# Kernel tuning notes

Hardware: AMD Instinct MI355X
Metric: run time of the kernel (lower is better)

The kernel has to match this reference:

```python
import jax, jax.numpy as jnp
import numpy as np

N = 50000      # ncount
IN_CH = 256    # in_channels
OUT_CH = 128   # out_channels
NNZ = 800000   # nnz per sparse matrix (avg degree 16)


def _spmm(rows, cols, vals, dense, n_rows):
    # sparse(COO) @ dense : gather rows of dense by col index, scale, scatter-add by row
    contrib = vals[:, None] * dense[cols]              # [nnz, F]
    return jax.ops.segment_sum(contrib, rows, num_segments=n_rows)


def setup_inputs() -> dict:
    key = jax.random.key(0)
    ks = jax.random.split(key, 12)
    phi_indices = jnp.stack([
        jax.random.randint(ks[0], (NNZ,), 0, N),
        jax.random.randint(ks[1], (NNZ,), 0, N)])
    phi_values = jax.random.normal(ks[2], (NNZ,), dtype=jnp.float32)
    phi_inverse_indices = jnp.stack([
        jax.random.randint(ks[3], (NNZ,), 0, N),
        jax.random.randint(ks[4], (NNZ,), 0, N)])
    phi_inverse_values = jax.random.normal(ks[5], (NNZ,), dtype=jnp.float32)
    feature_indices = jnp.stack([
        jax.random.randint(ks[6], (NNZ,), 0, N),       # node index
        jax.random.randint(ks[7], (NNZ,), 0, IN_CH)])  # feature column
    feature_values = jax.random.normal(ks[8], (NNZ,), dtype=jnp.float32)
    # xavier_uniform for weight_matrix
    limit = float(np.sqrt(6.0 / (IN_CH + OUT_CH)))
    weight_matrix = jax.random.uniform(ks[9], (IN_CH, OUT_CH), jnp.float32, -limit, limit)
    # diagonal filter Theta init uniform(0.9, 1.1)
    diagonal_weight_filter = jax.random.uniform(ks[10], (N,), jnp.float32, 0.9, 1.1)
    return {
        "phi_indices": phi_indices,
        "phi_values": phi_values,
        "phi_inverse_indices": phi_inverse_indices,
        "phi_inverse_values": phi_inverse_values,
        "feature_indices": feature_indices,
        "feature_values": feature_values,
        "weight_matrix": weight_matrix,
        "diagonal_weight_filter": diagonal_weight_filter,
        "dropout": 0,
    }


def reference(phi_indices, phi_values, phi_inverse_indices, phi_inverse_values,
              feature_indices, feature_values, weight_matrix,
              diagonal_weight_filter, dropout):
    # rescaled_phi = phi @ diag(theta): scales column j of phi by theta[j]
    scaled_phi_vals = phi_values * diagonal_weight_filter[phi_indices[1]]
    # filtered = features(sparse N x IN) @ W  -> [N, OUT]
    filtered = _spmm(feature_indices[0], feature_indices[1], feature_values,
                     weight_matrix, N)
    # (phi * D * phi_inv) @ filtered computed associatively without dense N x N:
    tmp = _spmm(phi_inverse_indices[0], phi_inverse_indices[1],
                phi_inverse_values, filtered, N)              # phi_inv @ filtered
    localized = _spmm(phi_indices[0], phi_indices[1],
                      scaled_phi_vals, tmp, N)                # (phi D) @ tmp
    # dropout in eval mode (training=False) is identity
    return jax.nn.relu(localized)
```

## Files before the change

### kernel.cpp

```cpp
#include <hip/hip_runtime.h>
#include <hip/hip_fp16.h>


#define OUT_CH 128
#define HALF_CH 64
#define RPB 256
#define RPB_SHIFT 8
#define MAX_NB 256
#define EPB 4096
#define MAX_CHUNK 16


__global__ __launch_bounds__(256) void bucket_hist_kernel(
    const int* __restrict__ rows0, int n0,
    const int* __restrict__ rows1, int n1,
    const int* __restrict__ rows2, int n2,
    int* __restrict__ hist_part,
    int NB, int NBLK)
{
    int m = blockIdx.y;
    const int* rows = (m == 0) ? rows0 : (m == 1) ? rows1 : rows2;
    int nnz         = (m == 0) ? n0    : (m == 1) ? n1    : n2;
    __shared__ int bins[MAX_NB];
    if (threadIdx.x < NB) bins[threadIdx.x] = 0;
    __syncthreads();
    int base = blockIdx.x * EPB;
    #pragma unroll 4
    for (int k = 0; k < EPB / 256; ++k) {
        int i = base + k * 256 + threadIdx.x;
        if (i < nnz) atomicAdd(&bins[rows[i] >> RPB_SHIFT], 1);
    }
    __syncthreads();
    int* out = hist_part + ((size_t)(m * NBLK + blockIdx.x)) * NB;
    if (threadIdx.x < NB) out[threadIdx.x] = bins[threadIdx.x];
}


__global__ __launch_bounds__(256) void scan_blocks_wave_kernel(
    int* __restrict__ hist_part, int* __restrict__ totals, int NB, int NBLK)
{
    int w = blockIdx.x * 4 + (threadIdx.x >> 6);
    if (w >= 3 * NB) return;
    int lane = threadIdx.x & 63;
    int m = w / NB, b = w - m * NB;
    const int chunk = (NBLK + 63) >> 6;
    int base_blk = lane * chunk;

    int v[MAX_CHUNK];
    int sum = 0;
    for (int k = 0; k < chunk; ++k) {
        int blk = base_blk + k;
        int x = (blk < NBLK) ? hist_part[((size_t)(m * NBLK + blk)) * NB + b] : 0;
        v[k] = x; sum += x;
    }
    int incl = sum;
    #pragma unroll
    for (int s = 1; s < 64; s <<= 1) {
        int y = __shfl_up(incl, s);
        if (lane >= s) incl += y;
    }
    int run = incl - sum;
    for (int k = 0; k < chunk; ++k) {
        int blk = base_blk + k;
        if (blk < NBLK) {
            hist_part[((size_t)(m * NBLK + blk)) * NB + b] = run;
            run += v[k];
        }
    }
    if (lane == 63) totals[w] = incl;
}


__global__ __launch_bounds__(1024) void scan_buckets_kernel(
    const int* __restrict__ totals, int* __restrict__ bases, int NB)
{
    int m = blockIdx.x;
    int t = threadIdx.x;
    int x = (t < NB) ? totals[m * NB + t] : 0;
    int lane = t & 63, wid = t >> 6;
    int incl = x;
    #pragma unroll
    for (int s = 1; s < 64; s <<= 1) {
        int y = __shfl_up(incl, s);
        if (lane >= s) incl += y;
    }
    __shared__ int wtot[16];
    __shared__ int wbase[16];
    if (lane == 63) wtot[wid] = incl;
    __syncthreads();
    if (t == 0) {
        int run = 0;
        #pragma unroll
        for (int w = 0; w < 16; ++w) { int v = wtot[w]; wbase[w] = run; run += v; }
    }
    __syncthreads();
    if (t < NB) bases[m * NB + t] = wbase[wid] + incl - x;
}


__global__ __launch_bounds__(256) void bucket_scatter_kernel(
    const int* __restrict__ rows0, const int* __restrict__ cols0, const float* __restrict__ vals0, int n0,
    const int* __restrict__ rows1, const int* __restrict__ cols1, const float* __restrict__ vals1, int n1,
    const int* __restrict__ rows2, const int* __restrict__ cols2, const float* __restrict__ vals2, int n2,
    const float* __restrict__ theta,
    const int* __restrict__ hist_part, const int* __restrict__ bases,
    int2* __restrict__ eb0, int2* __restrict__ eb1, int2* __restrict__ eb2,
    int NB, int NBLK)
{
    int m = blockIdx.y;
    const int* rows; const int* cols; const float* vals; int nnz; int2* eb;
    if (m == 0)      { rows = rows0; cols = cols0; vals = vals0; nnz = n0; eb = eb0; }
    else if (m == 1) { rows = rows1; cols = cols1; vals = vals1; nnz = n1; eb = eb1; }
    else             { rows = rows2; cols = cols2; vals = vals2; nnz = n2; eb = eb2; }

    __shared__ int cur[MAX_NB];
    const int* hp = hist_part + ((size_t)(m * NBLK + blockIdx.x)) * NB;
    const int* bs = bases + m * NB;
    if (threadIdx.x < NB) cur[threadIdx.x] = bs[threadIdx.x] + hp[threadIdx.x];
    __syncthreads();

    int base = blockIdx.x * EPB;
    bool fold = (m == 2);
    #pragma unroll 4
    for (int k = 0; k < EPB / 256; ++k) {
        int i = base + k * 256 + threadIdx.x;
        if (i < nnz) {
            int r = rows[i], c = cols[i];
            float v = vals[i];
            if (fold) v *= theta[c];
            int pos = atomicAdd(&cur[r >> RPB_SHIFT], 1);
            eb[pos] = make_int2(c | ((r & (RPB - 1)) << 16), __float_as_int(v));
        }
    }
}


__global__ __launch_bounds__(256) void bucket_to_csr_kernel(
    const int2* __restrict__ eb0, const int2* __restrict__ eb1, const int2* __restrict__ eb2,
    int2* __restrict__ ec0, int2* __restrict__ ec1, int2* __restrict__ ec2,
    const int* __restrict__ bases,
    int* __restrict__ off,
    int n0, int n1, int n2, int NB, int n)
{
    int m = blockIdx.y;
    int b = blockIdx.x;
    const int2* eb; int2* ec; int nnz;
    if (m == 0)      { eb = eb0; ec = ec0; nnz = n0; }
    else if (m == 1) { eb = eb1; ec = ec1; nnz = n1; }
    else             { eb = eb2; ec = ec2; nnz = n2; }
    int base = bases[m * NB + b];
    int end  = (b + 1 < NB) ? bases[m * NB + b + 1] : nnz;

    __shared__ int hist[RPB];
    __shared__ int cur[RPB];
    __shared__ int loc[RPB + 1];
    __shared__ int wtot[4];
    __shared__ int wbase[4];
    int t = threadIdx.x;
    hist[t] = 0; cur[t] = 0;
    __syncthreads();
    for (int i = base + t; i < end; i += 256)
        atomicAdd(&hist[(eb[i].x >> 16) & (RPB - 1)], 1);
    __syncthreads();
    {
        int x = hist[t];
        int lane = t & 63, wid = t >> 6;
        int incl = x;
        #pragma unroll
        for (int s = 1; s < 64; s <<= 1) {
            int y = __shfl_up(incl, s);
            if (lane >= s) incl += y;
        }
        if (lane == 63) wtot[wid] = incl;
        __syncthreads();
        if (t == 0) {
            int run = 0;
            #pragma unroll
            for (int w = 0; w < 4; ++w) { int v = wtot[w]; wbase[w] = run; run += v; }
        }
        __syncthreads();
        loc[t] = wbase[wid] + incl - x;
        if (t == RPB - 1) loc[RPB] = wbase[3] + incl;
    }
    __syncthreads();
    {
        int r = b * RPB + t;
        if (r <= n) off[(size_t)m * (n + 1) + r] = base + loc[t];
        if (b == NB - 1 && t == 0) off[(size_t)m * (n + 1) + n] = nnz;
    }
    for (int i = base + t; i < end; i += 256) {
        int2 e = eb[i];
        int rl = (e.x >> 16) & (RPB - 1);
        int rk = atomicAdd(&cur[rl], 1);
        ec[base + loc[rl] + rk] = make_int2(e.x & 0xFFFF, e.y);
    }
}


template<bool SRC_H, bool DST_H, bool RELU>
__global__ __launch_bounds__(256) void spmm_csr_kernel(
    const int* __restrict__ off, const int2* __restrict__ edges,
    const void* __restrict__ dense_v, void* __restrict__ out_v, int nrows)
{
    int lane = threadIdx.x & 63;
    int r = blockIdx.x * 4 + (threadIdx.x >> 6);
    if (r >= nrows) return;
    int j   = __builtin_amdgcn_readfirstlane(off[r]);
    int end = __builtin_amdgcn_readfirstlane(off[r + 1]);
    const float2*  df = (const float2*)dense_v;
    const __half2* dh = (const __half2*)dense_v;

    float2 a0 = make_float2(0.f, 0.f), a1 = make_float2(0.f, 0.f);

    for (; j + 4 <= end; j += 4) {
        int2 e0 = edges[j], e1 = edges[j + 1], e2 = edges[j + 2], e3 = edges[j + 3];
        float2 d0, d1, dd2, d3;
        if (SRC_H) {
            d0  = __half22float2(dh[(size_t)e0.x * HALF_CH + lane]);
            d1  = __half22float2(dh[(size_t)e1.x * HALF_CH + lane]);
            dd2 = __half22float2(dh[(size_t)e2.x * HALF_CH + lane]);
            d3  = __half22float2(dh[(size_t)e3.x * HALF_CH + lane]);
        } else {
            d0  = df[(size_t)e0.x * HALF_CH + lane];
            d1  = df[(size_t)e1.x * HALF_CH + lane];
            dd2 = df[(size_t)e2.x * HALF_CH + lane];
            d3  = df[(size_t)e3.x * HALF_CH + lane];
        }
        float v0 = __int_as_float(e0.y), v1 = __int_as_float(e1.y);
        float v2 = __int_as_float(e2.y), v3 = __int_as_float(e3.y);
        a0.x = fmaf(v0, d0.x, a0.x); a0.y = fmaf(v0, d0.y, a0.y);
        a1.x = fmaf(v1, d1.x, a1.x); a1.y = fmaf(v1, d1.y, a1.y);
        a0.x = fmaf(v2, dd2.x, a0.x); a0.y = fmaf(v2, dd2.y, a0.y);
        a1.x = fmaf(v3, d3.x, a1.x); a1.y = fmaf(v3, d3.y, a1.y);
    }
    for (; j < end; ++j) {
        int2 e0 = edges[j];
        float2 d0;
        if (SRC_H) d0 = __half22float2(dh[(size_t)e0.x * HALF_CH + lane]);
        else       d0 = df[(size_t)e0.x * HALF_CH + lane];
        float v0 = __int_as_float(e0.y);
        a0.x = fmaf(v0, d0.x, a0.x); a0.y = fmaf(v0, d0.y, a0.y);
    }
    float2 res = make_float2(a0.x + a1.x, a0.y + a1.y);
    if (RELU) { res.x = fmaxf(res.x, 0.f); res.y = fmaxf(res.y, 0.f); }
    if (DST_H) ((__half2*)out_v)[(size_t)r * HALF_CH + lane] = __float22half2_rn(res);
    else       ((float2*) out_v)[(size_t)r * HALF_CH + lane] = res;
}


__global__ __launch_bounds__(256) void spmm_atomic_kernel(
    const int* __restrict__ rows, const int* __restrict__ cols,
    const float* __restrict__ vals, const float* __restrict__ theta,
    const float* __restrict__ dense, float* __restrict__ out, int nnz)
{
    int idx = blockIdx.x * blockDim.x + threadIdx.x;
    int e = idx >> 7;
    int f = idx & (OUT_CH - 1);
    if (e >= nnz) return;
    int r = rows[e];
    int c = cols[e];
    float v = vals[e];
    if (theta != nullptr) v *= theta[c];
    atomicAdd(&out[(size_t)r * OUT_CH + f], v * dense[(size_t)c * OUT_CH + f]);
}

__global__ __launch_bounds__(256) void relu_kernel(float* __restrict__ out, int n4)
{
    int i = blockIdx.x * blockDim.x + threadIdx.x;
    if (i >= n4) return;
    float4 v = ((float4*)out)[i];
    v.x = fmaxf(v.x, 0.f); v.y = fmaxf(v.y, 0.f);
    v.z = fmaxf(v.z, 0.f); v.w = fmaxf(v.w, 0.f);
    ((float4*)out)[i] = v;
}


static inline size_t align16(size_t x) { return (x + 15) & ~(size_t)15; }

extern "C" void kernel_launch(void* const* d_in, const int* in_sizes, int n_in,
                              void* d_out, int out_size, void* d_ws, size_t ws_size,
                              hipStream_t stream)
{
    const int*   phi_idx   = (const int*)d_in[0];
    const float* phi_vals  = (const float*)d_in[1];
    const int*   phii_idx  = (const int*)d_in[2];
    const float* phii_vals = (const float*)d_in[3];
    const int*   feat_idx  = (const int*)d_in[4];
    const float* feat_vals = (const float*)d_in[5];
    const float* W         = (const float*)d_in[6];
    const float* theta     = (const float*)d_in[7];

    const int nnz_phi  = in_sizes[1];
    const int nnz_phii = in_sizes[3];
    const int nnz_feat = in_sizes[5];
    const int n_nodes  = in_sizes[7];
    const int in_ch    = in_sizes[6] / OUT_CH;
    const size_t dense_elems = (size_t)n_nodes * OUT_CH;
    const long long total_e = (long long)nnz_feat + nnz_phii + nnz_phi;

    const int NB = (n_nodes + RPB - 1) >> RPB_SHIFT;
    int max_nnz = nnz_feat > nnz_phii ? nnz_feat : nnz_phii;
    if (nnz_phi > max_nnz) max_nnz = nnz_phi;
    const int NBLK = (max_nnz + EPB - 1) / EPB;

    size_t p = 0;
    size_t filtered_off = p; p += align16(dense_elems * sizeof(__half));
    size_t tmp_off      = p; p += align16(dense_elems * sizeof(__half));
    size_t off_off      = p; p += align16((size_t)3 * (n_nodes + 1) * sizeof(int));
    size_t hp_off       = p; p += align16((size_t)3 * NBLK * NB * sizeof(int));
    size_t tot_off      = p; p += align16((size_t)3 * NB * sizeof(int));
    size_t bas_off      = p; p += align16((size_t)3 * NB * sizeof(int));
    size_t eb_off       = p; p += align16((size_t)total_e * sizeof(int2));
    size_t ec_off       = p; p += align16((size_t)total_e * sizeof(int2));
    size_t need = p;

    char* ws = (char*)d_ws;
    dim3 block(256);

    bool fast_ok = (ws_size >= need) && (NB <= MAX_NB) && (n_nodes <= 65536) &&
                   (in_ch <= 65536) && (NBLK <= 64 * MAX_CHUNK);

    if (fast_ok) {
        __half* filtered = (__half*)(ws + filtered_off);
        __half* tmp      = (__half*)(ws + tmp_off);
        int* off_arr    = (int*)(ws + off_off);
        int* hist_part  = (int*)(ws + hp_off);
        int* totals     = (int*)(ws + tot_off);
        int* bases      = (int*)(ws + bas_off);
        int2* eb0 = (int2*)(ws + eb_off);
        int2* eb1 = eb0 + nnz_feat;
        int2* eb2 = eb1 + nnz_phii;
        int2* ec0 = (int2*)(ws + ec_off);
        int2* ec1 = ec0 + nnz_feat;
        int2* ec2 = ec1 + nnz_phii;

        const int* rows0 = feat_idx;  const int* cols0 = feat_idx + nnz_feat;
        const int* rows1 = phii_idx;  const int* cols1 = phii_idx + nnz_phii;
        const int* rows2 = phi_idx;   const int* cols2 = phi_idx  + nnz_phi;

        bucket_hist_kernel<<<dim3(NBLK, 3), block, 0, stream>>>(
            rows0, nnz_feat, rows1, nnz_phii, rows2, nnz_phi,
            hist_part, NB, NBLK);

        int nwaves = 3 * NB;
        scan_blocks_wave_kernel<<<dim3((nwaves + 3) / 4), block, 0, stream>>>(
            hist_part, totals, NB, NBLK);

        scan_buckets_kernel<<<dim3(3), dim3(1024), 0, stream>>>(totals, bases, NB);

        bucket_scatter_kernel<<<dim3(NBLK, 3), block, 0, stream>>>(
            rows0, cols0, feat_vals, nnz_feat,
            rows1, cols1, phii_vals, nnz_phii,
            rows2, cols2, phi_vals,  nnz_phi,
            theta, hist_part, bases, eb0, eb1, eb2, NB, NBLK);

        bucket_to_csr_kernel<<<dim3(NB, 3), block, 0, stream>>>(
            eb0, eb1, eb2, ec0, ec1, ec2, bases, off_arr,
            nnz_feat, nnz_phii, nnz_phi, NB, n_nodes);

        int* off_f  = off_arr;
        int* off_pi = off_arr + (n_nodes + 1);
        int* off_p  = off_arr + 2 * (n_nodes + 1);

        dim3 grid_r((unsigned)((n_nodes + 3) / 4));
        spmm_csr_kernel<false, true, false><<<grid_r, block, 0, stream>>>(
            off_f,  ec0, (const void*)W, (void*)filtered, n_nodes);
        spmm_csr_kernel<true, true, false><<<grid_r, block, 0, stream>>>(
            off_pi, ec1, (const void*)filtered, (void*)tmp, n_nodes);
        spmm_csr_kernel<true, false, true><<<grid_r, block, 0, stream>>>(
            off_p,  ec2, (const void*)tmp, d_out, n_nodes);
    } else {
        float* filtered = (float*)ws;
        float* tmp      = filtered + dense_elems;
        hipMemsetAsync(filtered, 0, 2 * dense_elems * sizeof(float), stream);
        hipMemsetAsync(d_out, 0, (size_t)out_size * sizeof(float), stream);
        {
            long long t = (long long)nnz_feat * OUT_CH;
            spmm_atomic_kernel<<<dim3((unsigned)((t + 255) / 256)), block, 0, stream>>>(
                feat_idx, feat_idx + nnz_feat, feat_vals, nullptr, W, filtered, nnz_feat);
        }
        {
            long long t = (long long)nnz_phii * OUT_CH;
            spmm_atomic_kernel<<<dim3((unsigned)((t + 255) / 256)), block, 0, stream>>>(
                phii_idx, phii_idx + nnz_phii, phii_vals, nullptr, filtered, tmp, nnz_phii);
        }
        {
            long long t = (long long)nnz_phi * OUT_CH;
            spmm_atomic_kernel<<<dim3((unsigned)((t + 255) / 256)), block, 0, stream>>>(
                phi_idx, phi_idx + nnz_phi, phi_vals, theta, tmp, (float*)d_out, nnz_phi);
        }
        {
            int n4 = out_size / 4;
            relu_kernel<<<dim3((n4 + 255) / 256), block, 0, stream>>>((float*)d_out, n4);
        }
    }
}
```

Measured before the change: 251.9 us.

## Stage bucket scatter in shared memory and unroll SpMM gathers by eight

```diff
diff --git a/kernel.cpp b/kernel.cpp
--- a/kernel.cpp
+++ b/kernel.cpp
@@ -8,6 +8,7 @@
 #define RPB_SHIFT 8
 #define MAX_NB 256
 #define EPB 4096
+#define EPT 16
 #define MAX_CHUNK 16
 
 
@@ -113,24 +114,80 @@
     else if (m == 1) { rows = rows1; cols = cols1; vals = vals1; nnz = n1; eb = eb1; }
     else             { rows = rows2; cols = cols2; vals = vals2; nnz = n2; eb = eb2; }
 
-    __shared__ int cur[MAX_NB];
-    const int* hp = hist_part + ((size_t)(m * NBLK + blockIdx.x)) * NB;
-    const int* bs = bases + m * NB;
-    if (threadIdx.x < NB) cur[threadIdx.x] = bs[threadIdx.x] + hp[threadIdx.x];
+    __shared__ int2 staged[EPB];
+    __shared__ unsigned char bucket_of[EPB];
+    __shared__ int lhist[MAX_NB];
+    __shared__ int lstart[MAX_NB + 1];
+    __shared__ int lcur[MAX_NB];
+    __shared__ int gbase[MAX_NB];
+    __shared__ int wtot[4], wbase[4];
+
+    int t = threadIdx.x;
+    if (t < NB) lhist[t] = 0;
     __syncthreads();
 
     int base = blockIdx.x * EPB;
     bool fold = (m == 2);
-    #pragma unroll 4
-    for (int k = 0; k < EPB / 256; ++k) {
-        int i = base + k * 256 + threadIdx.x;
+
+    int  bk[EPT];
+    int2 pl[EPT];
+    #pragma unroll
+    for (int k = 0; k < EPT; ++k) {
+        int i = base + k * 256 + t;
         if (i < nnz) {
             int r = rows[i], c = cols[i];
             float v = vals[i];
             if (fold) v *= theta[c];
-            int pos = atomicAdd(&cur[r >> RPB_SHIFT], 1);
-            eb[pos] = make_int2(c | ((r & (RPB - 1)) << 16), __float_as_int(v));
-        }
+            bk[k] = r >> RPB_SHIFT;
+            pl[k] = make_int2(c | ((r & (RPB - 1)) << 16), __float_as_int(v));
+            atomicAdd(&lhist[bk[k]], 1);
+        } else bk[k] = -1;
+    }
+    __syncthreads();
+
+    {
+        int x = (t < NB) ? lhist[t] : 0;
+        int lane = t & 63, wid = t >> 6;
+        int incl = x;
+        #pragma unroll
+        for (int s = 1; s < 64; s <<= 1) {
+            int y = __shfl_up(incl, s);
+            if (lane >= s) incl += y;
+        }
+        if (lane == 63) wtot[wid] = incl;
+        __syncthreads();
+        if (t == 0) {
+            int run = 0;
+            #pragma unroll
+            for (int w = 0; w < 4; ++w) { int v = wtot[w]; wbase[w] = run; run += v; }
+            lstart[MAX_NB] = run;
+        }
+        __syncthreads();
+        if (t < NB) {
+            int excl = wbase[wid] + incl - x;
+            lstart[t] = excl;
+            lcur[t]   = excl;
+            const int* hp = hist_part + ((size_t)(m * NBLK + blockIdx.x)) * NB;
+            gbase[t] = bases[m * NB + t] + hp[t];
+        }
+    }
+    __syncthreads();
+
+    #pragma unroll
+    for (int k = 0; k < EPT; ++k) {
+        if (bk[k] >= 0) {
+            int idx = atomicAdd(&lcur[bk[k]], 1);
+            staged[idx] = pl[k];
+            bucket_of[idx] = (unsigned char)bk[k];
+        }
+    }
+    __syncthreads();
+
+    int count = min(EPB, nnz - base);
+    for (int i = t; i < count; i += 256) {
+        int b = bucket_of[i];
+        int dest = gbase[b] + (i - lstart[b]);
+        eb[dest] = staged[i];
     }
 }
 
@@ -212,26 +269,37 @@
 
     float2 a0 = make_float2(0.f, 0.f), a1 = make_float2(0.f, 0.f);
 
+    for (; j + 8 <= end; j += 8) {
+        int2 e[8]; float2 d[8];
+        #pragma unroll
+        for (int k = 0; k < 8; ++k) e[k] = edges[j + k];
+        #pragma unroll
+        for (int k = 0; k < 8; ++k) {
+            if (SRC_H) d[k] = __half22float2(dh[(size_t)e[k].x * HALF_CH + lane]);
+            else       d[k] = df[(size_t)e[k].x * HALF_CH + lane];
+        }
+        #pragma unroll
+        for (int k = 0; k < 8; ++k) {
+            float v = __int_as_float(e[k].y);
+            if (k & 1) { a1.x = fmaf(v, d[k].x, a1.x); a1.y = fmaf(v, d[k].y, a1.y); }
+            else       { a0.x = fmaf(v, d[k].x, a0.x); a0.y = fmaf(v, d[k].y, a0.y); }
+        }
+    }
     for (; j + 4 <= end; j += 4) {
-        int2 e0 = edges[j], e1 = edges[j + 1], e2 = edges[j + 2], e3 = edges[j + 3];
-        float2 d0, d1, dd2, d3;
-        if (SRC_H) {
-            d0  = __half22float2(dh[(size_t)e0.x * HALF_CH + lane]);
-            d1  = __half22float2(dh[(size_t)e1.x * HALF_CH + lane]);
-            dd2 = __half22float2(dh[(size_t)e2.x * HALF_CH + lane]);
-            d3  = __half22float2(dh[(size_t)e3.x * HALF_CH + lane]);
-        } else {
-            d0  = df[(size_t)e0.x * HALF_CH + lane];
-            d1  = df[(size_t)e1.x * HALF_CH + lane];
-            dd2 = df[(size_t)e2.x * HALF_CH + lane];
-            d3  = df[(size_t)e3.x * HALF_CH + lane];
-        }
-        float v0 = __int_as_float(e0.y), v1 = __int_as_float(e1.y);
-        float v2 = __int_as_float(e2.y), v3 = __int_as_float(e3.y);
-        a0.x = fmaf(v0, d0.x, a0.x); a0.y = fmaf(v0, d0.y, a0.y);
-        a1.x = fmaf(v1, d1.x, a1.x); a1.y = fmaf(v1, d1.y, a1.y);
-        a0.x = fmaf(v2, dd2.x, a0.x); a0.y = fmaf(v2, dd2.y, a0.y);
-        a1.x = fmaf(v3, d3.x, a1.x); a1.y = fmaf(v3, d3.y, a1.y);
+        int2 e[4]; float2 d[4];
+        #pragma unroll
+        for (int k = 0; k < 4; ++k) e[k] = edges[j + k];
+        #pragma unroll
+        for (int k = 0; k < 4; ++k) {
+            if (SRC_H) d[k] = __half22float2(dh[(size_t)e[k].x * HALF_CH + lane]);
+            else       d[k] = df[(size_t)e[k].x * HALF_CH + lane];
+        }
+        #pragma unroll
+        for (int k = 0; k < 4; ++k) {
+            float v = __int_as_float(e[k].y);
+            if (k & 1) { a1.x = fmaf(v, d[k].x, a1.x); a1.y = fmaf(v, d[k].y, a1.y); }
+            else       { a0.x = fmaf(v, d[k].x, a0.x); a0.y = fmaf(v, d[k].y, a0.y); }
+        }
     }
     for (; j < end; ++j) {
         int2 e0 = edges[j];
```

Result: faster. 228.1 us, median of 2 (-9.4%).
